# Optimization experiments

Measured on AMD Instinct MI355X. Metric: run time of the kernel, lower is better.

Reference implementation:

```python
import jax, jax.numpy as jnp
import numpy as np

N_NODES = 50000
N_EDGES = 800000
D_IN = 64
D_OUT = 64


def setup_inputs() -> dict:
    key = jax.random.key(0)
    k1, k2, k3, k4, k5 = jax.random.split(key, 5)
    features = jax.random.normal(k1, (N_NODES, D_IN), dtype=jnp.float32)
    edge_src = jax.random.randint(k2, (N_EDGES,), 0, N_NODES, dtype=jnp.int32)
    edge_dst = jax.random.randint(k3, (N_EDGES,), 0, N_NODES, dtype=jnp.int32)
    edge_weight = jax.random.uniform(k4, (N_EDGES,), dtype=jnp.float32)
    # Linear(2*D_IN, D_OUT): weight [D_OUT, 2*D_IN], bias [D_OUT]
    W = jax.random.normal(k5, (D_OUT, 2 * D_IN), dtype=jnp.float32) * (1.0 / np.sqrt(2 * D_IN))
    b = jnp.zeros((D_OUT,), dtype=jnp.float32)
    return {"features": features, "edge_src": edge_src, "edge_dst": edge_dst,
            "edge_weight": edge_weight, "W": W, "b": b}


def reference(features, edge_src, edge_dst, edge_weight, W, b):
    n = features.shape[0]
    # spmm(adj, features): out[i] = sum_j adj[i,j] * features[j]
    gathered = features[edge_src] * edge_weight[:, None]          # [E, D_IN]
    neighbor = jax.ops.segment_sum(gathered, edge_dst, num_segments=n)  # [N, D_IN]
    combined = jnp.concatenate([features, neighbor], axis=1)     # [N, 2*D_IN]
    out = combined @ W.T + b                                      # [N, D_OUT]
    # F.normalize(p=2, dim=1): x / max(||x||, 1e-12)
    norm = jnp.maximum(jnp.linalg.norm(out, axis=1, keepdims=True), 1e-12)
    return out / norm
```

## Files before the change

### kernel.cpp

```cpp
#include <hip/hip_runtime.h>

#define D 64
#define TILE 1024
#define RB 8
#define EPB 2048
#define EPT 8

__global__ __launch_bounds__(256) void hist_kernel(
    const int* __restrict__ edge_dst, int* __restrict__ deg,
    int n_edges, int n_nodes)
{
    __shared__ int s_cnt;
    __shared__ int s_d[EPB];
    int r = blockIdx.x & (RB - 1);
    int chunk = blockIdx.x >> 3;
    int lo = (int)((long long)r * n_nodes / RB);
    int hi = (int)((long long)(r + 1) * n_nodes / RB);
    if (threadIdx.x == 0) s_cnt = 0;
    __syncthreads();

    int base = chunk * EPB + threadIdx.x * EPT;
    int d[EPT];
    if (base + EPT - 1 < n_edges) {
        int4 v0 = *(const int4*)(edge_dst + base);
        int4 v1 = *(const int4*)(edge_dst + base + 4);
        d[0]=v0.x; d[1]=v0.y; d[2]=v0.z; d[3]=v0.w;
        d[4]=v1.x; d[5]=v1.y; d[6]=v1.z; d[7]=v1.w;
    } else {
        #pragma unroll
        for (int k = 0; k < EPT; ++k)
            d[k] = (base + k < n_edges) ? edge_dst[base + k] : -1;
    }

    int lane = threadIdx.x & 63;
    unsigned long long lt = (lane == 63) ? ~0ull >> 1
                                         : ((1ull << (lane + 1)) - 1) >> 1;
    #pragma unroll
    for (int k = 0; k < EPT; ++k) {
        bool m = (d[k] >= lo && d[k] < hi);
        unsigned long long bal = __ballot(m);
        int cw = __popcll(bal);
        if (cw) {
            int bs = 0;
            if (lane == 0) bs = atomicAdd(&s_cnt, cw);
            bs = __builtin_amdgcn_readfirstlane(bs);
            if (m) s_d[bs + __popcll(bal & lt)] = d[k];
        }
    }
    __syncthreads();
    int c = s_cnt;
    for (int i = threadIdx.x; i < c; i += 256) atomicAdd(&deg[s_d[i]], 1);
}

__global__ __launch_bounds__(256) void tile_sum_kernel(
    const int* __restrict__ deg, int* __restrict__ partial, int n)
{
    int t = threadIdx.x;
    int base = blockIdx.x * TILE + t * 4;
    int s = 0;
    if (base + 3 < n) {
        int4 v = *(const int4*)(deg + base);
        s = v.x + v.y + v.z + v.w;
    } else {
        for (int k = 0; k < 4; ++k) if (base + k < n) s += deg[base + k];
    }
    #pragma unroll
    for (int off = 1; off < 64; off <<= 1) s += __shfl_xor(s, off, 64);
    __shared__ int wsum[4];
    int lane = t & 63, wv = t >> 6;
    if (lane == 0) wsum[wv] = s;
    __syncthreads();
    if (t == 0) partial[blockIdx.x] = wsum[0] + wsum[1] + wsum[2] + wsum[3];
}

__global__ __launch_bounds__(64) void scan_partial_kernel(
    const int* __restrict__ partial, int* __restrict__ ppref, int nb,
    int* __restrict__ offsets, int n, int n_edges)
{
    int lane = threadIdx.x;
    int carry = 0;
    for (int base = 0; base < nb; base += 64) {
        int idx = base + lane;
        int v = (idx < nb) ? partial[idx] : 0;
        int inc = v;
        #pragma unroll
        for (int off = 1; off < 64; off <<= 1) {
            int u = __shfl_up(inc, off, 64);
            if (lane >= off) inc += u;
        }
        if (idx < nb) ppref[idx] = carry + inc - v;
        carry += __shfl(inc, 63, 64);
    }
    if (lane == 0) offsets[n] = n_edges;
}

__global__ __launch_bounds__(256) void scan_tile_kernel(
    const int* __restrict__ deg, const int* __restrict__ ppref,
    int* __restrict__ offsets, int* __restrict__ cursor, int n)
{
    int t = threadIdx.x;
    int base = blockIdx.x * TILE + t * 4;
    int e0 = 0, e1 = 0, e2 = 0, e3 = 0;
    if (base + 3 < n) {
        int4 v = *(const int4*)(deg + base);
        e0 = v.x; e1 = v.y; e2 = v.z; e3 = v.w;
    } else {
        if (base + 0 < n) e0 = deg[base + 0];
        if (base + 1 < n) e1 = deg[base + 1];
        if (base + 2 < n) e2 = deg[base + 2];
        if (base + 3 < n) e3 = deg[base + 3];
    }
    int s = e0 + e1 + e2 + e3;
    int inc = s;
    int lane = t & 63, wv = t >> 6;
    #pragma unroll
    for (int off = 1; off < 64; off <<= 1) {
        int u = __shfl_up(inc, off, 64);
        if (lane >= off) inc += u;
    }
    __shared__ int wsum[4];
    if (lane == 63) wsum[wv] = inc;
    __syncthreads();
    int wpre = 0;
    for (int wq = 0; wq < wv; ++wq) wpre += wsum[wq];
    int excl = ppref[blockIdx.x] + wpre + inc - s;
    int o0 = excl, o1 = o0 + e0, o2 = o1 + e1, o3 = o2 + e2;
    if (base + 0 < n) { offsets[base + 0] = o0; cursor[base + 0] = o0; }
    if (base + 1 < n) { offsets[base + 1] = o1; cursor[base + 1] = o1; }
    if (base + 2 < n) { offsets[base + 2] = o2; cursor[base + 2] = o2; }
    if (base + 3 < n) { offsets[base + 3] = o3; cursor[base + 3] = o3; }
}

__global__ __launch_bounds__(256) void fill_kernel(
    const int* __restrict__ edge_src, const int* __restrict__ edge_dst,
    const float* __restrict__ edge_weight,
    int* __restrict__ cursor, int2* __restrict__ csr_sw,
    int n_edges, int n_nodes)
{
    __shared__ int s_cnt;
    __shared__ int s_d[EPB];
    __shared__ int s_e[EPB];
    int r = blockIdx.x & (RB - 1);
    int chunk = blockIdx.x >> 3;
    int lo = (int)((long long)r * n_nodes / RB);
    int hi = (int)((long long)(r + 1) * n_nodes / RB);
    if (threadIdx.x == 0) s_cnt = 0;
    __syncthreads();

    int base = chunk * EPB + threadIdx.x * EPT;
    int d[EPT];
    if (base + EPT - 1 < n_edges) {
        int4 v0 = *(const int4*)(edge_dst + base);
        int4 v1 = *(const int4*)(edge_dst + base + 4);
        d[0]=v0.x; d[1]=v0.y; d[2]=v0.z; d[3]=v0.w;
        d[4]=v1.x; d[5]=v1.y; d[6]=v1.z; d[7]=v1.w;
    } else {
        #pragma unroll
        for (int k = 0; k < EPT; ++k)
            d[k] = (base + k < n_edges) ? edge_dst[base + k] : -1;
    }

    int lane = threadIdx.x & 63;
    unsigned long long lt = (lane == 63) ? ~0ull >> 1
                                         : ((1ull << (lane + 1)) - 1) >> 1;
    #pragma unroll
    for (int k = 0; k < EPT; ++k) {
        bool m = (d[k] >= lo && d[k] < hi);
        unsigned long long bal = __ballot(m);
        int cw = __popcll(bal);
        if (cw) {
            int bs = 0;
            if (lane == 0) bs = atomicAdd(&s_cnt, cw);
            bs = __builtin_amdgcn_readfirstlane(bs);
            if (m) {
                int p = bs + __popcll(bal & lt);
                s_d[p] = d[k];
                s_e[p] = base + k;
            }
        }
    }
    __syncthreads();
    int c = s_cnt;
    for (int i = threadIdx.x; i < c; i += 256) {
        int dk = s_d[i];
        int e  = s_e[i];
        int pos = atomicAdd(&cursor[dk], 1);
        csr_sw[pos] = make_int2(edge_src[e], __float_as_int(edge_weight[e]));
    }
}

__global__ __launch_bounds__(256) void gather_kernel(
    const float* __restrict__ features, const int2* __restrict__ csr_sw,
    const int* __restrict__ offsets, float* __restrict__ neighbor, int n_nodes)
{
    int lane = threadIdx.x & 63;
    int gw = (blockIdx.x * 256 + threadIdx.x) >> 6;
    int nw = (gridDim.x * 256) >> 6;
    for (int i = gw; i < n_nodes; i += nw) {
        int beg = __builtin_amdgcn_readfirstlane(offsets[i]);
        int end = __builtin_amdgcn_readfirstlane(offsets[i + 1]);
        float acc = 0.f;
        int j = beg;
        for (; j + 7 < end; j += 8) {
            int2 p[8];
            float a[8];
            #pragma unroll
            for (int q = 0; q < 8; ++q) p[q] = csr_sw[j + q];
            #pragma unroll
            for (int q = 0; q < 8; ++q)
                a[q] = features[(size_t)p[q].x * D + lane];
            #pragma unroll
            for (int q = 0; q < 8; ++q)
                acc = fmaf(__int_as_float(p[q].y), a[q], acc);
        }
        for (; j < end; ++j) {
            int2 p = csr_sw[j];
            acc = fmaf(__int_as_float(p.y), features[(size_t)p.x * D + lane], acc);
        }
        neighbor[(size_t)i * D + lane] = acc;
    }
}

__global__ __launch_bounds__(256) void gemm_norm_kernel(
    const float* __restrict__ features, const float* __restrict__ neighbor,
    const float* __restrict__ W, const float* __restrict__ bias,
    float* __restrict__ out, int n_nodes)
{
    __shared__ float4 Wt4[32][64];
    __shared__ float comb[4][8][128];
    int tid = threadIdx.x;
    for (int idx = tid; idx < 32 * 64; idx += 256) {
        int k4 = idx >> 6, o = idx & 63;
        Wt4[k4][o] = *(const float4*)(W + (size_t)o * 128 + k4 * 4);
    }
    __syncthreads();

    int lane = tid & 63;
    int wv = tid >> 6;
    float bl = bias[lane];

    int ngroups = (n_nodes + 7) >> 3;
    for (int g = blockIdx.x * 4 + wv; g < ngroups; g += gridDim.x * 4) {
        int i0 = g * 8;
        int cnt = min(8, n_nodes - i0);

        #pragma unroll
        for (int t = 0; t < 8; ++t) {
            int i = i0 + ((t < cnt) ? t : 0);
            comb[wv][t][lane]      = features[(size_t)i * D + lane];
            comb[wv][t][64 + lane] = neighbor[(size_t)i * D + lane];
        }

        float acc[8];
        #pragma unroll
        for (int t = 0; t < 8; ++t) acc[t] = bl;

        #pragma unroll 4
        for (int k4 = 0; k4 < 32; ++k4) {
            float4 w4 = Wt4[k4][lane];
            #pragma unroll
            for (int t = 0; t < 8; ++t) {
                float4 c4 = *(const float4*)&comb[wv][t][4 * k4];
                acc[t] = fmaf(c4.x, w4.x, acc[t]);
                acc[t] = fmaf(c4.y, w4.y, acc[t]);
                acc[t] = fmaf(c4.z, w4.z, acc[t]);
                acc[t] = fmaf(c4.w, w4.w, acc[t]);
            }
        }

        #pragma unroll
        for (int t = 0; t < 8; ++t) {
            if (t < cnt) {
                float s = acc[t] * acc[t];
                #pragma unroll
                for (int m = 1; m < 64; m <<= 1) s += __shfl_xor(s, m, 64);
                out[(size_t)(i0 + t) * D + lane] =
                    acc[t] / fmaxf(sqrtf(s), 1e-12f);
            }
        }
    }
}

extern "C" void kernel_launch(void* const* d_in, const int* in_sizes, int n_in,
                              void* d_out, int out_size, void* d_ws, size_t ws_size,
                              hipStream_t stream) {
    const float* features    = (const float*)d_in[0];
    const int*   edge_src    = (const int*)d_in[1];
    const int*   edge_dst    = (const int*)d_in[2];
    const float* edge_weight = (const float*)d_in[3];
    const float* W           = (const float*)d_in[4];
    const float* b           = (const float*)d_in[5];
    float*       out         = (float*)d_out;

    int n = in_sizes[0] / D;
    int E = in_sizes[1];
    int nb = (n + TILE - 1) / TILE;
    int nchunks = (E + EPB - 1) / EPB;

    char* ws = (char*)d_ws;
    auto al = [](size_t x) { return (x + 255) & ~(size_t)255; };
    size_t o = 0;
    int* deg      = (int*)(ws + o); o += al((size_t)n * 4);
    int* cursor   = (int*)(ws + o); o += al((size_t)n * 4);
    int* offsets  = (int*)(ws + o); o += al((size_t)(n + 1) * 4);
    int* partial  = (int*)(ws + o); o += al((size_t)nb * 4);
    int* ppref    = (int*)(ws + o); o += al((size_t)nb * 4);
    int2* csr_sw  = (int2*)(ws + o); o += al((size_t)E * 8);
    float* neighbor = (float*)(ws + o);

    hipMemsetAsync(deg, 0, (size_t)n * 4, stream);

    hist_kernel<<<nchunks * RB, 256, 0, stream>>>(edge_dst, deg, E, n);
    tile_sum_kernel<<<nb, 256, 0, stream>>>(deg, partial, n);
    scan_partial_kernel<<<1, 64, 0, stream>>>(partial, ppref, nb, offsets, n, E);
    scan_tile_kernel<<<nb, 256, 0, stream>>>(deg, ppref, offsets, cursor, n);
    fill_kernel<<<nchunks * RB, 256, 0, stream>>>(edge_src, edge_dst, edge_weight,
                                                  cursor, csr_sw, E, n);
    gather_kernel<<<2048, 256, 0, stream>>>(features, csr_sw, offsets,
                                            neighbor, n);
    gemm_norm_kernel<<<512, 256, 0, stream>>>(features, neighbor, W, b, out, n);
}
```

Baseline: 228.4 us.

## Register-tile the dense GEMM+normalize with pre-transposed W in LDS

Replaces the wave-per-8-nodes GEMM, which staged inputs through shared memory, with a 64-thread block computing a 64x64 output tile. Each thread holds an 8x8 register tile and reads features/neighbor rows directly as float4 from global memory. A separate small kernel transposes W once so blocks can copy it into LDS with contiguous float4 loads. The aim is to cut LDS traffic per FMA and raise arithmetic intensity, at the cost of an extra launch, a 32KB LDS reload per small block, and higher register pressure.

```diff
diff --git a/kernel.cpp b/kernel.cpp
--- a/kernel.cpp
+++ b/kernel.cpp
@@ -221,62 +221,110 @@
     }
 }
 
-__global__ __launch_bounds__(256) void gemm_norm_kernel(
+__global__ __launch_bounds__(128) void wtrans_kernel(
+    const float* __restrict__ W, float* __restrict__ Wt)
+{
+    int idx = blockIdx.x * 128 + threadIdx.x;
+    if (idx < 64 * 128) {
+        int o = idx >> 7, k = idx & 127;
+        Wt[k * 64 + o] = W[idx];
+    }
+}
+
+__global__ __launch_bounds__(64) void gemm_norm_kernel(
     const float* __restrict__ features, const float* __restrict__ neighbor,
-    const float* __restrict__ W, const float* __restrict__ bias,
+    const float* __restrict__ Wt,
+    const float* __restrict__ bias,
     float* __restrict__ out, int n_nodes)
 {
-    __shared__ float4 Wt4[32][64];
-    __shared__ float comb[4][8][128];
+    __shared__ float Wl[128 * 64];
     int tid = threadIdx.x;
-    for (int idx = tid; idx < 32 * 64; idx += 256) {
-        int k4 = idx >> 6, o = idx & 63;
-        Wt4[k4][o] = *(const float4*)(W + (size_t)o * 128 + k4 * 4);
-    }
-    __syncthreads();
-
-    int lane = tid & 63;
-    int wv = tid >> 6;
-    float bl = bias[lane];
-
-    int ngroups = (n_nodes + 7) >> 3;
-    for (int g = blockIdx.x * 4 + wv; g < ngroups; g += gridDim.x * 4) {
-        int i0 = g * 8;
-        int cnt = min(8, n_nodes - i0);
-
-        #pragma unroll
-        for (int t = 0; t < 8; ++t) {
-            int i = i0 + ((t < cnt) ? t : 0);
-            comb[wv][t][lane]      = features[(size_t)i * D + lane];
-            comb[wv][t][64 + lane] = neighbor[(size_t)i * D + lane];
-        }
-
-        float acc[8];
-        #pragma unroll
-        for (int t = 0; t < 8; ++t) acc[t] = bl;
-
-        #pragma unroll 4
-        for (int k4 = 0; k4 < 32; ++k4) {
-            float4 w4 = Wt4[k4][lane];
+    {
+        const float4* src = (const float4*)Wt;
+        float4* dst = (float4*)Wl;
+        #pragma unroll
+        for (int i = 0; i < 32; ++i) dst[tid + i * 64] = src[tid + i * 64];
+    }
+    __syncthreads();
+
+    int nt = tid & 7;
+    int mt = tid >> 3;
+
+    long long i0 = (long long)blockIdx.x * 64;
+
+    int nclamp[8];
+    #pragma unroll
+    for (int t = 0; t < 8; ++t) {
+        long long node = i0 + mt + 8 * t;
+        nclamp[t] = (int)((node < n_nodes) ? node : (n_nodes - 1));
+    }
+
+    float acc[8][8];
+    #pragma unroll
+    for (int t = 0; t < 8; ++t)
+        #pragma unroll
+        for (int j = 0; j < 8; ++j) acc[t][j] = 0.f;
+
+    #pragma unroll
+    for (int h = 0; h < 2; ++h) {
+        const float* __restrict__ A = (h == 0) ? features : neighbor;
+        #pragma unroll 1
+        for (int k4 = 0; k4 < 16; ++k4) {
+            float4 a4[8];
+            #pragma unroll
+            for (int t = 0; t < 8; ++t)
+                a4[t] = *(const float4*)(A + (size_t)nclamp[t] * D + k4 * 4);
+            int kk = h * 64 + k4 * 4;
+            float4 b0[4], b1[4];
+            #pragma unroll
+            for (int i = 0; i < 4; ++i) {
+                const float* wrow = Wl + (kk + i) * 64 + nt * 8;
+                b0[i] = *(const float4*)(wrow);
+                b1[i] = *(const float4*)(wrow + 4);
+            }
             #pragma unroll
             for (int t = 0; t < 8; ++t) {
-                float4 c4 = *(const float4*)&comb[wv][t][4 * k4];
-                acc[t] = fmaf(c4.x, w4.x, acc[t]);
-                acc[t] = fmaf(c4.y, w4.y, acc[t]);
-                acc[t] = fmaf(c4.z, w4.z, acc[t]);
-                acc[t] = fmaf(c4.w, w4.w, acc[t]);
+                float av[4] = {a4[t].x, a4[t].y, a4[t].z, a4[t].w};
+                #pragma unroll
+                for (int i = 0; i < 4; ++i) {
+                    acc[t][0] = fmaf(av[i], b0[i].x, acc[t][0]);
+                    acc[t][1] = fmaf(av[i], b0[i].y, acc[t][1]);
+                    acc[t][2] = fmaf(av[i], b0[i].z, acc[t][2]);
+                    acc[t][3] = fmaf(av[i], b0[i].w, acc[t][3]);
+                    acc[t][4] = fmaf(av[i], b1[i].x, acc[t][4]);
+                    acc[t][5] = fmaf(av[i], b1[i].y, acc[t][5]);
+                    acc[t][6] = fmaf(av[i], b1[i].z, acc[t][6]);
+                    acc[t][7] = fmaf(av[i], b1[i].w, acc[t][7]);
+                }
             }
         }
-
-        #pragma unroll
-        for (int t = 0; t < 8; ++t) {
-            if (t < cnt) {
-                float s = acc[t] * acc[t];
-                #pragma unroll
-                for (int m = 1; m < 64; m <<= 1) s += __shfl_xor(s, m, 64);
-                out[(size_t)(i0 + t) * D + lane] =
-                    acc[t] / fmaxf(sqrtf(s), 1e-12f);
-            }
+    }
+
+    float bl[8];
+    #pragma unroll
+    for (int j = 0; j < 8; ++j) bl[j] = bias[nt * 8 + j];
+
+    #pragma unroll
+    for (int t = 0; t < 8; ++t) {
+        long long node = i0 + mt + 8 * t;
+        float s = 0.f;
+        #pragma unroll
+        for (int j = 0; j < 8; ++j) {
+            acc[t][j] += bl[j];
+            s = fmaf(acc[t][j], acc[t][j], s);
+        }
+        s += __shfl_xor(s, 1, 64);
+        s += __shfl_xor(s, 2, 64);
+        s += __shfl_xor(s, 4, 64);
+        float inv = 1.f / fmaxf(sqrtf(s), 1e-12f);
+        if (node < n_nodes) {
+            float4 o0 = make_float4(acc[t][0] * inv, acc[t][1] * inv,
+                                    acc[t][2] * inv, acc[t][3] * inv);
+            float4 o1 = make_float4(acc[t][4] * inv, acc[t][5] * inv,
+                                    acc[t][6] * inv, acc[t][7] * inv);
+            float* op = out + (size_t)node * D + nt * 8;
+            *(float4*)op = o0;
+            *(float4*)(op + 4) = o1;
         }
     }
 }
@@ -305,11 +353,13 @@
     int* offsets  = (int*)(ws + o); o += al((size_t)(n + 1) * 4);
     int* partial  = (int*)(ws + o); o += al((size_t)nb * 4);
     int* ppref    = (int*)(ws + o); o += al((size_t)nb * 4);
+    float* Wt     = (float*)(ws + o); o += al((size_t)64 * 128 * 4);
     int2* csr_sw  = (int2*)(ws + o); o += al((size_t)E * 8);
     float* neighbor = (float*)(ws + o);
 
     hipMemsetAsync(deg, 0, (size_t)n * 4, stream);
 
+    wtrans_kernel<<<64, 128, 0, stream>>>(W, Wt);
     hist_kernel<<<nchunks * RB, 256, 0, stream>>>(edge_dst, deg, E, n);
     tile_sum_kernel<<<nb, 256, 0, stream>>>(deg, partial, n);
     scan_partial_kernel<<<1, 64, 0, stream>>>(partial, ppref, nb, offsets, n, E);
@@ -318,5 +368,7 @@
                                                   cursor, csr_sw, E, n);
     gather_kernel<<<2048, 256, 0, stream>>>(features, csr_sw, offsets,
                                             neighbor, n);
-    gemm_norm_kernel<<<512, 256, 0, stream>>>(features, neighbor, W, b, out, n);
-}
+    int gblocks = (n + 63) / 64;
+    gemm_norm_kernel<<<gblocks, 64, 0, stream>>>(features, neighbor, Wt, b,
+                                                 out, n);
+}
```

New measurement: 215.8 us. 1.06x faster.
